# Kernel tuning notes

Hardware: AMD Instinct MI355X
Metric: run time of the kernel (lower is better)

## Reference

```python
import jax, jax.numpy as jnp
import numpy as np

B, C, W, H = 4, 256, 64, 64

def setup_inputs() -> dict:
    key = jax.random.key(0)
    ks = jax.random.split(key, 6)
    return {
        "fm_source": jax.random.normal(ks[0], (B, C, W, H), dtype=jnp.float32),
        "fm_reference": jax.random.normal(ks[1], (B, C, W, H), dtype=jnp.float32),
        "w_lambda": jax.random.normal(ks[2], (1, C, 1, 1), dtype=jnp.float32) * 0.05,
        "b_lambda": jax.random.normal(ks[3], (1,), dtype=jnp.float32) * 0.05,
        "w_beta": jax.random.normal(ks[4], (1, C, 1, 1), dtype=jnp.float32) * 0.05,
        "b_beta": jax.random.normal(ks[5], (1,), dtype=jnp.float32) * 0.05,
    }

def reference(fm_source, fm_reference, w_lambda, b_lambda, w_beta, b_beta):
    b, c, w, h = fm_reference.shape
    n = w * h
    # 1x1 convs on the reference feature map -> per-pixel scalars, flattened to [B, N]
    wl = w_lambda.reshape(c)
    wb = w_beta.reshape(c)
    ref_flat = fm_reference.reshape(b, c, n)   # [B, C, N]
    src_flat = fm_source.reshape(b, c, n)      # [B, C, N]
    old_lambda = jnp.einsum("bcn,c->bn", ref_flat, wl) + b_lambda[0]  # [B, N]
    old_beta = jnp.einsum("bcn,c->bn", ref_flat, wb) + b_beta[0]      # [B, N]
    # energy[b, i, j] = <src pixel i, ref pixel j> over channels
    energy = jnp.einsum("bci,bcj->bij", src_flat, ref_flat)  # [B, N, N]
    attention = jax.nn.softmax(energy, axis=-1)              # softmax over ref pixels j
    # new_lambda[b, i] = sum_j old_lambda[b, j] * attention[b, i, j]
    new_lambda = jnp.einsum("bj,bij->bi", old_lambda, attention).reshape(b, 1, w, h)
    new_beta = jnp.einsum("bj,bij->bi", old_beta, attention).reshape(b, 1, w, h)
    # broadcast modulation over the 256 channels
    return new_lambda * fm_source + new_beta
```

## Files before the change

kernel.cpp:

```cpp
#include <hip/hip_runtime.h>


#define B_ 4
#define C_ 256
#define N_ 4096
#define LOG2E 1.44269504f
#define SHIFT2 86.5617f
#define JSLICE 4
#define BN_ (B_ * N_)
#define NT_ 32
#define PH_ 8

typedef _Float16 half_t;
typedef _Float16 v8h  __attribute__((ext_vector_type(8)));
typedef float    v16f __attribute__((ext_vector_type(16)));

#define GLDS16(g, l) __builtin_amdgcn_global_load_lds(                         \
    (const __attribute__((address_space(1))) void*)(g),                        \
    (__attribute__((address_space(3))) void*)(l), 16, 0, 0)

__global__ void k_prep(const float* __restrict__ ref,
                       const float* __restrict__ wl,
                       const float* __restrict__ wb,
                       half_t* __restrict__ r16,
                       float* __restrict__ oldL, float* __restrict__ oldB) {
    __shared__ float tile[64][65];
    __shared__ float red[8][64];
    int b  = blockIdx.z;
    int c0 = blockIdx.y * 64;
    int n0 = blockIdx.x * 64;
    int tid = threadIdx.x;
    int tx = tid & 15, ty = tid >> 4;
#pragma unroll
    for (int q = 0; q < 4; q++) {
        int c = ty + q * 16;
        float4 v = *(const float4*)(ref + ((size_t)b * C_ + c0 + c) * N_ + n0 + tx * 4);
        tile[c][tx * 4 + 0] = v.x;
        tile[c][tx * 4 + 1] = v.y;
        tile[c][tx * 4 + 2] = v.z;
        tile[c][tx * 4 + 3] = v.w;
    }
    __syncthreads();
    int r   = tid & 31;
    int lhi = (tid >> 5) & 1;
    int wv  = tid >> 6;
#pragma unroll
    for (int nt = 0; nt < 2; nt++) {
        int nl = nt * 32 + r;
        v8h o;
#pragma unroll
        for (int e = 0; e < 8; e++)
            o[e] = (half_t)tile[wv * 16 + lhi * 8 + e][nl];
        size_t tj = (size_t)(n0 >> 5) + nt;
        size_t kb = (size_t)(c0 >> 4) + wv;
        *(v8h*)(r16 + ((((size_t)b * 128 + tj) * 16 + kb) * 64 + (tid & 63)) * 8) = o;
    }
    int n  = tid & 63;
    int cq = tid >> 6;
    float aL = 0.f, aB = 0.f;
#pragma unroll
    for (int c = 0; c < 16; c++) {
        float v = tile[cq * 16 + c][n];
        aL += v * wl[c0 + cq * 16 + c];
        aB += v * wb[c0 + cq * 16 + c];
    }
    red[cq][n]     = aL;
    red[4 + cq][n] = aB;
    __syncthreads();
    if (tid < 64) {
        atomicAdd(&oldL[(size_t)b * N_ + n0 + tid],
                  red[0][tid] + red[1][tid] + red[2][tid] + red[3][tid]);
    } else if (tid < 128) {
        int u = tid - 64;
        atomicAdd(&oldB[(size_t)b * N_ + n0 + u],
                  red[4][u] + red[5][u] + red[6][u] + red[7][u]);
    }
}

__global__ __launch_bounds__(512, 2) void k_flash(
        const float* __restrict__ src, const half_t* __restrict__ rT,
        const float* __restrict__ oldL, const float* __restrict__ oldB,
        const float* __restrict__ bl, const float* __restrict__ bb,
        float* __restrict__ sumP, float* __restrict__ sumL,
        float* __restrict__ sumB) {
    __shared__ half_t lds[2][32768];
    int bid    = blockIdx.x;
    int b      = bid & 3;
    int jslice = (bid >> 2) & (JSLICE - 1);
    int iblock = bid >> 4;
    int tid    = threadIdx.x;
    int wv     = tid >> 6;
    int lane   = tid & 63;
    int l31    = lane & 31, lhi = lane >> 5;
    int ti     = iblock * 8 + wv;
    int i0     = ti * 32;
    int j0     = jslice * (N_ / JSLICE);
    int tj0    = j0 >> 5;

    const float* aS = src + (size_t)b * C_ * N_ + i0 + l31;
    v8h a[16];
#pragma unroll
    for (int kb = 0; kb < 16; kb++) {
        v8h o;
#pragma unroll
        for (int e = 0; e < 8; e++)
            o[e] = (half_t)(aS[(size_t)(kb * 16 + lhi * 8 + e) * N_] * LOG2E);
        a[kb] = o;
    }

    const half_t* bBase = rT + (((size_t)b * 128 + tj0) * 16) * 512;
    const float*  oLp = oldL + (size_t)b * N_ + j0 + l31;
    const float*  oBp = oldB + (size_t)b * N_ + j0 + l31;
    float bl0 = bl[0], bb0 = bb[0];

    float sp[16], sl[16], sb[16];
#pragma unroll
    for (int r = 0; r < 16; r++) { sp[r] = 0.f; sl[r] = 0.f; sb[r] = 0.f; }

#pragma unroll
    for (int q = 0; q < 8; q++) {
        int chunk = q * 8 + wv;
        GLDS16(bBase + (size_t)chunk * 512 + (size_t)lane * 8,
               &lds[0][(size_t)chunk * 512]);
    }

    for (int ph = 0; ph < PH_; ph++) {
        __syncthreads();
        if (ph + 1 < PH_) {
            const half_t* g = bBase + (size_t)(ph + 1) * 32768;
#pragma unroll
            for (int q = 0; q < 8; q++) {
                int chunk = q * 8 + wv;
                GLDS16(g + (size_t)chunk * 512 + (size_t)lane * 8,
                       &lds[(ph + 1) & 1][(size_t)chunk * 512]);
            }
        }
        float lamv[4], betv[4];
#pragma unroll
        for (int t = 0; t < 4; t++) {
            lamv[t] = oLp[(ph * 4 + t) * 32] + bl0;
            betv[t] = oBp[(ph * 4 + t) * 32] + bb0;
        }
        const half_t* btb = lds[ph & 1] + (size_t)lane * 8;
#pragma unroll
        for (int t = 0; t < 4; t++) {
            const half_t* bt = btb + (size_t)t * 8192;
            v16f acc0, acc1;
#pragma unroll
            for (int r = 0; r < 16; r++) { acc0[r] = -SHIFT2; acc1[r] = 0.f; }
#pragma unroll
            for (int kb = 0; kb < 8; kb++) {
                acc0 = __builtin_amdgcn_mfma_f32_32x32x16_f16(
                    a[kb],     *(const v8h*)(bt + (size_t)kb * 512),       acc0, 0, 0, 0);
                acc1 = __builtin_amdgcn_mfma_f32_32x32x16_f16(
                    a[kb + 8], *(const v8h*)(bt + (size_t)(kb + 8) * 512), acc1, 0, 0, 0);
            }
            float lam = lamv[t], bet = betv[t];
#pragma unroll
            for (int r = 0; r < 16; r++) {
                float p = __builtin_amdgcn_exp2f(acc0[r] + acc1[r]);
                sp[r] += p;
                sl[r] += p * lam;
                sb[r] += p * bet;
            }
        }
    }

#pragma unroll
    for (int r = 0; r < 16; r++) {
        float tp = sp[r], tl = sl[r], tb = sb[r];
#pragma unroll
        for (int m = 1; m <= 16; m <<= 1) {
            tp += __shfl_xor(tp, m, 64);
            tl += __shfl_xor(tl, m, 64);
            tb += __shfl_xor(tb, m, 64);
        }
        if (l31 == 0) {
            int row = (r & 3) + 8 * (r >> 2) + 4 * lhi;
            size_t ig = (size_t)b * N_ + i0 + row;
            atomicAdd(&sumP[ig], tp);
            atomicAdd(&sumL[ig], tl);
            atomicAdd(&sumB[ig], tb);
        }
    }
}

__global__ void k_post(const float* __restrict__ src,
                       const float* __restrict__ sumP,
                       const float* __restrict__ sumL,
                       const float* __restrict__ sumB,
                       float* __restrict__ out) {
    int b  = blockIdx.x;
    int n0 = blockIdx.y * 1024;
    int c0 = blockIdx.z * 16;
    int t  = threadIdx.x;
    size_t bn = (size_t)b * N_ + n0 + t * 4;
    float4 sp = *(const float4*)(sumP + bn);
    float4 sl = *(const float4*)(sumL + bn);
    float4 sb = *(const float4*)(sumB + bn);
    float4 L, T;
    L.x = sl.x / sp.x; L.y = sl.y / sp.y; L.z = sl.z / sp.z; L.w = sl.w / sp.w;
    T.x = sb.x / sp.x; T.y = sb.y / sp.y; T.z = sb.z / sp.z; T.w = sb.w / sp.w;
    const float* sp0 = src + ((size_t)b * C_ + c0) * N_ + n0 + t * 4;
    float*       op0 = out + ((size_t)b * C_ + c0) * N_ + n0 + t * 4;
#pragma unroll 4
    for (int c = 0; c < 16; c++) {
        float4 v = *(const float4*)(sp0 + (size_t)c * N_);
        float4 o;
        o.x = L.x * v.x + T.x;
        o.y = L.y * v.y + T.y;
        o.z = L.z * v.z + T.z;
        o.w = L.w * v.w + T.w;
        *(float4*)(op0 + (size_t)c * N_) = o;
    }
}

extern "C" void kernel_launch(void* const* d_in, const int* in_sizes, int n_in,
                              void* d_out, int out_size, void* d_ws, size_t ws_size,
                              hipStream_t stream) {
    const float* src = (const float*)d_in[0];
    const float* ref = (const float*)d_in[1];
    const float* wl  = (const float*)d_in[2];
    const float* bl  = (const float*)d_in[3];
    const float* wb  = (const float*)d_in[4];
    const float* bb  = (const float*)d_in[5];
    float* out = (float*)d_out;

    float* oldL = (float*)d_ws;
    float* oldB = oldL + BN_;
    float* sumP = oldB + BN_;
    float* sumL = sumP + BN_;
    float* sumB = sumL + BN_;
    size_t needF  = (size_t)5 * BN_ * sizeof(float);
    size_t need16 = (size_t)B_ * N_ * C_ * sizeof(half_t);
    half_t* r16;
    if (ws_size >= needF + need16) r16 = (half_t*)((char*)d_ws + needF);
    else                           r16 = (half_t*)d_out;

    hipMemsetAsync(d_ws, 0, needF, stream);
    k_prep<<<dim3(N_ / 64, C_ / 64, B_), 256, 0, stream>>>(
        ref, wl, wb, r16, oldL, oldB);
    k_flash<<<B_ * JSLICE * 16, 512, 0, stream>>>(
        src, r16, oldL, oldB, bl, bb, sumP, sumL, sumB);
    k_post<<<dim3(B_, N_ / 1024, C_ / 16), 256, 0, stream>>>(
        src, sumP, sumL, sumB, out);
}
```

Before: 145.8 us.

## Pre-pack source to fp16 MFMA layout, double j-slices, drop memset and atomics

The prep kernel now also converts the source feature map into the fp16 MFMA operand layout, pre-scaled by log2e. The flash kernel then loads its A operands as contiguous vectors instead of strided scalar fp32 loads. JSLICE is doubled and the LDS double buffer halved so more blocks run with a higher occupancy target. The memset is folded into the prep kernel, and the lambda/beta atomics are replaced by per-channel-block partial writes that the flash kernel sums. The post kernel also uses more, smaller blocks. In exchange, the extra fp16 source buffer costs bandwidth and workspace, and the flash kernel issues more atomics per output row.

```diff
diff --git a/kernel.cpp b/kernel.cpp
--- a/kernel.cpp
+++ b/kernel.cpp
@@ -6,9 +6,9 @@
 #define N_ 4096
 #define LOG2E 1.44269504f
 #define SHIFT2 86.5617f
-#define JSLICE 4
+#define JSLICE 8
 #define BN_ (B_ * N_)
-#define NT_ 32
+#define NT_ 16
 #define PH_ 8
 
 typedef _Float16 half_t;
@@ -19,22 +19,33 @@
     (const __attribute__((address_space(1))) void*)(g),                        \
     (__attribute__((address_space(3))) void*)(l), 16, 0, 0)
 
-__global__ void k_prep(const float* __restrict__ ref,
+__global__ void k_prep(const float* __restrict__ src,
+                       const float* __restrict__ ref,
                        const float* __restrict__ wl,
                        const float* __restrict__ wb,
-                       half_t* __restrict__ r16,
-                       float* __restrict__ oldL, float* __restrict__ oldB) {
+                       half_t* __restrict__ s16, half_t* __restrict__ r16,
+                       float* __restrict__ oldLp, float* __restrict__ oldBp,
+                       float* __restrict__ sums ) {
     __shared__ float tile[64][65];
     __shared__ float red[8][64];
-    int b  = blockIdx.z;
+    int z  = blockIdx.z;
+    int isRef = z >> 2;
+    int b  = z & 3;
+    const float* in  = isRef ? ref : src;
+    half_t*      out = isRef ? r16 : s16;
+    float scale      = isRef ? 1.0f : LOG2E;
     int c0 = blockIdx.y * 64;
     int n0 = blockIdx.x * 64;
     int tid = threadIdx.x;
+    if (z == 0) {
+        int gid = (blockIdx.y * 64 + blockIdx.x) * 256 + tid;
+        if (gid < 3 * BN_) sums[gid] = 0.f;
+    }
     int tx = tid & 15, ty = tid >> 4;
 #pragma unroll
     for (int q = 0; q < 4; q++) {
         int c = ty + q * 16;
-        float4 v = *(const float4*)(ref + ((size_t)b * C_ + c0 + c) * N_ + n0 + tx * 4);
+        float4 v = *(const float4*)(in + ((size_t)b * C_ + c0 + c) * N_ + n0 + tx * 4);
         tile[c][tx * 4 + 0] = v.x;
         tile[c][tx * 4 + 1] = v.y;
         tile[c][tx * 4 + 2] = v.z;
@@ -50,11 +61,12 @@
         v8h o;
 #pragma unroll
         for (int e = 0; e < 8; e++)
-            o[e] = (half_t)tile[wv * 16 + lhi * 8 + e][nl];
+            o[e] = (half_t)(tile[wv * 16 + lhi * 8 + e][nl] * scale);
         size_t tj = (size_t)(n0 >> 5) + nt;
         size_t kb = (size_t)(c0 >> 4) + wv;
-        *(v8h*)(r16 + ((((size_t)b * 128 + tj) * 16 + kb) * 64 + (tid & 63)) * 8) = o;
-    }
+        *(v8h*)(out + ((((size_t)b * 128 + tj) * 16 + kb) * 64 + (tid & 63)) * 8) = o;
+    }
+    if (!isRef) return;
     int n  = tid & 63;
     int cq = tid >> 6;
     float aL = 0.f, aB = 0.f;
@@ -67,27 +79,26 @@
     red[cq][n]     = aL;
     red[4 + cq][n] = aB;
     __syncthreads();
+    size_t slot = ((size_t)blockIdx.y * B_ + b) * N_ + n0;
     if (tid < 64) {
-        atomicAdd(&oldL[(size_t)b * N_ + n0 + tid],
-                  red[0][tid] + red[1][tid] + red[2][tid] + red[3][tid]);
+        oldLp[slot + tid] = red[0][tid] + red[1][tid] + red[2][tid] + red[3][tid];
     } else if (tid < 128) {
         int u = tid - 64;
-        atomicAdd(&oldB[(size_t)b * N_ + n0 + u],
-                  red[4][u] + red[5][u] + red[6][u] + red[7][u]);
-    }
-}
-
-__global__ __launch_bounds__(512, 2) void k_flash(
-        const float* __restrict__ src, const half_t* __restrict__ rT,
-        const float* __restrict__ oldL, const float* __restrict__ oldB,
+        oldBp[slot + u] = red[4][u] + red[5][u] + red[6][u] + red[7][u];
+    }
+}
+
+__global__ __launch_bounds__(512, 4) void k_flash(
+        const half_t* __restrict__ sT, const half_t* __restrict__ rT,
+        const float* __restrict__ oldLp, const float* __restrict__ oldBp,
         const float* __restrict__ bl, const float* __restrict__ bb,
         float* __restrict__ sumP, float* __restrict__ sumL,
         float* __restrict__ sumB) {
-    __shared__ half_t lds[2][32768];
+    __shared__ half_t lds[2][16384];
     int bid    = blockIdx.x;
     int b      = bid & 3;
     int jslice = (bid >> 2) & (JSLICE - 1);
-    int iblock = bid >> 4;
+    int iblock = bid >> 5;
     int tid    = threadIdx.x;
     int wv     = tid >> 6;
     int lane   = tid & 63;
@@ -97,20 +108,14 @@
     int j0     = jslice * (N_ / JSLICE);
     int tj0    = j0 >> 5;
 
-    const float* aS = src + (size_t)b * C_ * N_ + i0 + l31;
+    const half_t* aP = sT + (((size_t)b * 128 + ti) * 16) * 512 + (size_t)lane * 8;
     v8h a[16];
 #pragma unroll
-    for (int kb = 0; kb < 16; kb++) {
-        v8h o;
-#pragma unroll
-        for (int e = 0; e < 8; e++)
-            o[e] = (half_t)(aS[(size_t)(kb * 16 + lhi * 8 + e) * N_] * LOG2E);
-        a[kb] = o;
-    }
+    for (int kb = 0; kb < 16; kb++) a[kb] = *(const v8h*)(aP + (size_t)kb * 512);
 
     const half_t* bBase = rT + (((size_t)b * 128 + tj0) * 16) * 512;
-    const float*  oLp = oldL + (size_t)b * N_ + j0 + l31;
-    const float*  oBp = oldB + (size_t)b * N_ + j0 + l31;
+    const float*  oLp = oldLp + (size_t)b * N_ + j0 + l31;
+    const float*  oBp = oldBp + (size_t)b * N_ + j0 + l31;
     float bl0 = bl[0], bb0 = bb[0];
 
     float sp[16], sl[16], sb[16];
@@ -118,7 +123,7 @@
     for (int r = 0; r < 16; r++) { sp[r] = 0.f; sl[r] = 0.f; sb[r] = 0.f; }
 
 #pragma unroll
-    for (int q = 0; q < 8; q++) {
+    for (int q = 0; q < 4; q++) {
         int chunk = q * 8 + wv;
         GLDS16(bBase + (size_t)chunk * 512 + (size_t)lane * 8,
                &lds[0][(size_t)chunk * 512]);
@@ -127,24 +132,22 @@
     for (int ph = 0; ph < PH_; ph++) {
         __syncthreads();
         if (ph + 1 < PH_) {
-            const half_t* g = bBase + (size_t)(ph + 1) * 32768;
-#pragma unroll
-            for (int q = 0; q < 8; q++) {
+            const half_t* g = bBase + (size_t)(ph + 1) * 16384;
+#pragma unroll
+            for (int q = 0; q < 4; q++) {
                 int chunk = q * 8 + wv;
                 GLDS16(g + (size_t)chunk * 512 + (size_t)lane * 8,
                        &lds[(ph + 1) & 1][(size_t)chunk * 512]);
             }
         }
-        float lamv[4], betv[4];
-#pragma unroll
-        for (int t = 0; t < 4; t++) {
-            lamv[t] = oLp[(ph * 4 + t) * 32] + bl0;
-            betv[t] = oBp[(ph * 4 + t) * 32] + bb0;
-        }
-        const half_t* btb = lds[ph & 1] + (size_t)lane * 8;
-#pragma unroll
-        for (int t = 0; t < 4; t++) {
-            const half_t* bt = btb + (size_t)t * 8192;
+#pragma unroll
+        for (int t = 0; t < 2; t++) {
+            int jt = ph * 2 + t;
+            const half_t* bt = lds[ph & 1] + (size_t)t * 8192 + (size_t)lane * 8;
+            float lam = oLp[jt * 32]           + oLp[BN_ + jt * 32]
+                      + oLp[2 * BN_ + jt * 32] + oLp[3 * BN_ + jt * 32] + bl0;
+            float bet = oBp[jt * 32]           + oBp[BN_ + jt * 32]
+                      + oBp[2 * BN_ + jt * 32] + oBp[3 * BN_ + jt * 32] + bb0;
             v16f acc0, acc1;
 #pragma unroll
             for (int r = 0; r < 16; r++) { acc0[r] = -SHIFT2; acc1[r] = 0.f; }
@@ -155,7 +158,6 @@
                 acc1 = __builtin_amdgcn_mfma_f32_32x32x16_f16(
                     a[kb + 8], *(const v8h*)(bt + (size_t)(kb + 8) * 512), acc1, 0, 0, 0);
             }
-            float lam = lamv[t], bet = betv[t];
 #pragma unroll
             for (int r = 0; r < 16; r++) {
                 float p = __builtin_amdgcn_exp2f(acc0[r] + acc1[r]);
@@ -186,25 +188,23 @@
 }
 
 __global__ void k_post(const float* __restrict__ src,
-                       const float* __restrict__ sumP,
-                       const float* __restrict__ sumL,
-                       const float* __restrict__ sumB,
+                       const float* __restrict__ sums,
                        float* __restrict__ out) {
     int b  = blockIdx.x;
     int n0 = blockIdx.y * 1024;
-    int c0 = blockIdx.z * 16;
+    int c0 = blockIdx.z * 4;
     int t  = threadIdx.x;
     size_t bn = (size_t)b * N_ + n0 + t * 4;
-    float4 sp = *(const float4*)(sumP + bn);
-    float4 sl = *(const float4*)(sumL + bn);
-    float4 sb = *(const float4*)(sumB + bn);
+    float4 sp = *(const float4*)(sums + bn);
+    float4 sl = *(const float4*)(sums + BN_ + bn);
+    float4 sb = *(const float4*)(sums + 2 * BN_ + bn);
     float4 L, T;
     L.x = sl.x / sp.x; L.y = sl.y / sp.y; L.z = sl.z / sp.z; L.w = sl.w / sp.w;
     T.x = sb.x / sp.x; T.y = sb.y / sp.y; T.z = sb.z / sp.z; T.w = sb.w / sp.w;
     const float* sp0 = src + ((size_t)b * C_ + c0) * N_ + n0 + t * 4;
     float*       op0 = out + ((size_t)b * C_ + c0) * N_ + n0 + t * 4;
-#pragma unroll 4
-    for (int c = 0; c < 16; c++) {
+#pragma unroll
+    for (int c = 0; c < 4; c++) {
         float4 v = *(const float4*)(sp0 + (size_t)c * N_);
         float4 o;
         o.x = L.x * v.x + T.x;
@@ -226,22 +226,22 @@
     const float* bb  = (const float*)d_in[5];
     float* out = (float*)d_out;
 
-    float* oldL = (float*)d_ws;
-    float* oldB = oldL + BN_;
-    float* sumP = oldB + BN_;
-    float* sumL = sumP + BN_;
-    float* sumB = sumL + BN_;
-    size_t needF  = (size_t)5 * BN_ * sizeof(float);
-    size_t need16 = (size_t)B_ * N_ * C_ * sizeof(half_t);
-    half_t* r16;
-    if (ws_size >= needF + need16) r16 = (half_t*)((char*)d_ws + needF);
-    else                           r16 = (half_t*)d_out;
-
-    hipMemsetAsync(d_ws, 0, needF, stream);
-    k_prep<<<dim3(N_ / 64, C_ / 64, B_), 256, 0, stream>>>(
-        ref, wl, wb, r16, oldL, oldB);
+    float* oldLp = (float*)d_ws;
+    float* oldBp = oldLp + 4 * BN_;
+    float* sums  = oldBp + 4 * BN_;
+    float* sumP  = sums;
+    float* sumL  = sums + BN_;
+    float* sumB  = sums + 2 * BN_;
+    size_t needF  = (size_t)11 * BN_ * sizeof(float);
+    size_t need16 = (size_t)2 * B_ * N_ * C_ * sizeof(half_t);
+    half_t* s16;
+    if (ws_size >= needF + need16) s16 = (half_t*)((char*)d_ws + needF);
+    else                           s16 = (half_t*)d_out;
+    half_t* r16 = s16 + (size_t)B_ * N_ * C_;
+
+    k_prep<<<dim3(N_ / 64, C_ / 64, 8), 256, 0, stream>>>(
+        src, ref, wl, wb, s16, r16, oldLp, oldBp, sums);
     k_flash<<<B_ * JSLICE * 16, 512, 0, stream>>>(
-        src, r16, oldL, oldB, bl, bb, sumP, sumL, sumB);
-    k_post<<<dim3(B_, N_ / 1024, C_ / 16), 256, 0, stream>>>(
-        src, sumP, sumL, sumB, out);
-}
+        s16, r16, oldLp, oldBp, bl, bb, sumP, sumL, sumB);
+    k_post<<<dim3(B_, N_ / 1024, C_ / 4), 256, 0, stream>>>(src, sums, out);
+}
```

Result: slower. 385.9 us (+164.7%).
